# Performance work log

Measured on AMD Instinct MI355X. Metric: run time of the kernel, lower is better.

## Reference

```python
import jax, jax.numpy as jnp
import numpy as np

HEADS = 16
DIM_HEAD = 64


def setup_inputs() -> dict:
    key = jax.random.key(0)
    k1, k2, k3, k4, k5 = jax.random.split(key, 5)
    B, S, E = 4, 2048, 1024
    inner = HEADS * DIM_HEAD  # 1024
    return {
        "hidden_states": jax.random.normal(k1, (B, S, E), dtype=jnp.float32),
        "w_q": jax.random.normal(k2, (E, inner), dtype=jnp.float32) * (E ** -0.5),
        "w_k": jax.random.normal(k3, (E, inner), dtype=jnp.float32) * (E ** -0.5),
        "w_v": jax.random.normal(k4, (E, inner), dtype=jnp.float32) * (E ** -0.5),
        "w_o": jax.random.normal(k5, (inner, E), dtype=jnp.float32) * (inner ** -0.5),
    }


def reference(hidden_states, w_q, w_k, w_v, w_o):
    # Self-attention path: context = hidden_states (context arg is None).
    B, S, _ = hidden_states.shape
    dtype = hidden_states.dtype
    scale = DIM_HEAD ** -0.5

    q = (hidden_states @ w_q).reshape(B, S, HEADS, DIM_HEAD)
    k = (hidden_states @ w_k).reshape(B, S, HEADS, DIM_HEAD)
    v = (hidden_states @ w_v).reshape(B, S, HEADS, DIM_HEAD)

    # fp32 softmax as in the original module
    q32 = q.astype(jnp.float32)
    k32 = k.astype(jnp.float32)
    scores = jnp.einsum('btnh,bfnh->bnft', k32, q32) * scale  # [B, H, S_q, S_kv]
    probs = jax.nn.softmax(scores, axis=-1).astype(dtype)

    out = jnp.einsum('bnft,btnh->bfnh', probs, v)  # [B, S, H, D]
    out = out.reshape(B, S, HEADS * DIM_HEAD)
    return out @ w_o  # [B, S, query_dim]
```

## Files before the change

kernel.cpp:

```cpp
#include <hip/hip_runtime.h>
#include <stdint.h>

typedef __attribute__((ext_vector_type(8))) unsigned short ushort8;
typedef __attribute__((ext_vector_type(8))) __bf16 bf16x8;
typedef __attribute__((ext_vector_type(4))) float f32x4;
typedef __attribute__((ext_vector_type(4))) uint32_t u32x4;

#define TBK 32

__device__ __forceinline__ unsigned short f2bf(float f) {
  union { float f; uint32_t u; } x; x.f = f;
  uint32_t u = x.u;
  uint32_t r = (u + 0x7fffu + ((u >> 16) & 1u)) >> 16;
  return (unsigned short)r;
}

__device__ __forceinline__ uint32_t pack_bf2(float lo, float hi) {
  return (uint32_t)f2bf(lo) | ((uint32_t)f2bf(hi) << 16);
}

__device__ __forceinline__ uint32_t rhu2(float lo, float hi) {
  union { float f; uint32_t u; } a, b; a.f = lo; b.f = hi;
  return __builtin_amdgcn_perm(b.u + 0x8000u, a.u + 0x8000u, 0x07060302u);
}

__device__ __forceinline__ void store_c(unsigned short* p, float v) { *p = f2bf(v); }
__device__ __forceinline__ void store_c(float* p, float v) { *p = v; }

__device__ __forceinline__ void gll16(const unsigned short* g, unsigned short* l) {
  __builtin_amdgcn_global_load_lds((const __attribute__((address_space(1))) void*)g,
                                   (__attribute__((address_space(3))) void*)l,
                                   16, 0, 0);
}

__global__ __launch_bounds__(256) void cvt_f32_bf16(
    const float* __restrict__ x, unsigned short* __restrict__ y, int n4) {
  int i = blockIdx.x * 256 + threadIdx.x;
  if (i >= n4) return;
  float4 v = *(const float4*)(x + (size_t)i * 4);
  uint2 p; p.x = pack_bf2(v.x, v.y); p.y = pack_bf2(v.z, v.w);
  *(uint2*)(y + (size_t)i * 4) = p;
}

__global__ void transpose_w(const float* __restrict__ W,
                            unsigned short* __restrict__ WT) {
  __shared__ unsigned short tile[32][33];
  int c0 = blockIdx.x * 32, r0 = blockIdx.y * 32;
  int x = threadIdx.x, y = threadIdx.y;
#pragma unroll
  for (int i = 0; i < 32; i += 8)
    tile[y + i][x] = f2bf(W[(size_t)(r0 + y + i) * 1024 + c0 + x]);
  __syncthreads();
#pragma unroll
  for (int i = 0; i < 32; i += 8)
    WT[(size_t)(c0 + y + i) * 1024 + r0 + x] = tile[x][y + i];
}

template <typename OutT>
__global__ __launch_bounds__(256) void gemm_bt(
    const unsigned short* A,
    const unsigned short* BT0, const unsigned short* BT1, const unsigned short* BT2,
    OutT* C0, OutT* C1, OutT* C2,
    int M, int N, int K) {
  const unsigned short* BT = (blockIdx.z == 0) ? BT0 : (blockIdx.z == 1) ? BT1 : BT2;
  OutT* C = (blockIdx.z == 0) ? C0 : (blockIdx.z == 1) ? C1 : C2;

  __shared__ __attribute__((aligned(16))) unsigned short As[128 * TBK];
  __shared__ __attribute__((aligned(16))) unsigned short Bs[128 * TBK];

  const int tid = threadIdx.x;
  const int wave = tid >> 6, lane = tid & 63;
  const int fr = lane & 15, fq = lane >> 4;
  const int bm = blockIdx.x * 128, bn = blockIdx.y * 128;
  const int wm = (wave >> 1) * 64, wn = (wave & 1) * 64;

  f32x4 acc[4][4] = {};

  const int sr = lane >> 2;
  const int sk = (lane & 3) * 8;
  const unsigned short* Ag = A + (size_t)(bm + wave * 32 + sr) * K + sk;
  const unsigned short* Bg = BT + (size_t)(bn + wave * 32 + sr) * K + sk;
  unsigned short* As0 = &As[(wave * 32) * TBK];
  unsigned short* Bs0 = &Bs[(wave * 32) * TBK];

  for (int k0 = 0; k0 < K; k0 += TBK) {
    gll16(Ag + k0, As0);
    gll16(Ag + k0 + 16 * K, As0 + 16 * TBK);
    gll16(Bg + k0, Bs0);
    gll16(Bg + k0 + 16 * K, Bs0 + 16 * TBK);
    asm volatile("s_waitcnt vmcnt(0)" ::: "memory");
    __syncthreads();

    bf16x8 af[4], bfr[4];
#pragma unroll
    for (int mt = 0; mt < 4; mt++)
      af[mt] = *(const bf16x8*)&As[(wm + mt * 16 + fr) * TBK + fq * 8];
#pragma unroll
    for (int nt = 0; nt < 4; nt++)
      bfr[nt] = *(const bf16x8*)&Bs[(wn + nt * 16 + fr) * TBK + fq * 8];
#pragma unroll
    for (int mt = 0; mt < 4; mt++)
#pragma unroll
      for (int nt = 0; nt < 4; nt++)
        acc[mt][nt] = __builtin_amdgcn_mfma_f32_16x16x32_bf16(af[mt], bfr[nt], acc[mt][nt], 0, 0, 0);
    __syncthreads();
  }

#pragma unroll
  for (int mt = 0; mt < 4; mt++)
#pragma unroll
    for (int nt = 0; nt < 4; nt++)
#pragma unroll
      for (int r = 0; r < 4; r++) {
        int row = bm + wm + mt * 16 + fq * 4 + r;
        int col = bn + wn + nt * 16 + fr;
        store_c(&C[(size_t)row * N + col], acc[mt][nt][r]);
      }
}

#define SQ 72

__global__ __launch_bounds__(256, 4) void attn_kernel(
    const unsigned short* q, const unsigned short* k,
    const unsigned short* v, unsigned short* o) {
  const int S = 2048, E = 1024;
  __shared__ __attribute__((aligned(16))) unsigned short Ks[64 * SQ];
  __shared__ __attribute__((aligned(16))) unsigned short Vt[64 * SQ];

  const int tid = threadIdx.x;
  const int wave = tid >> 6, lane = tid & 63;
  const int fr = lane & 15, fq = lane >> 4;
  const int q0 = blockIdx.x * 128;
  const int bh = blockIdx.y;
  const int b = bh >> 4, h = bh & 15;
  const size_t base = ((size_t)b * S) * E + (size_t)h * 64;

  bf16x8 aq[2][2];
#pragma unroll
  for (int qg = 0; qg < 2; qg++)
#pragma unroll
    for (int ks = 0; ks < 2; ks++)
      aq[qg][ks] = *(const bf16x8*)&q[base +
          (size_t)(q0 + qg * 64 + wave * 16 + fr) * E + ks * 32 + fq * 8];

  ushort8 ones_u;
#pragma unroll
  for (int j = 0; j < 8; j++) ones_u[j] = 0x3F80;
  bf16x8 onesf = *(bf16x8*)&ones_u;

  f32x4 ot[2][4] = {};
  f32x4 osum[2] = {};
  const float KSC = 0.125f * 1.44269504088896341f;

  const int rp = (tid & 31) * 2;
  const int dcv = (tid >> 5) * 8;
  const int u_ = rp & 31;
  const int slot = 32 * (rp >> 5) + 8 * ((u_ & 15) >> 2) + 4 * (u_ >> 4) + (u_ & 3);

  for (int t0 = 0; t0 < S; t0 += 64) {
    __syncthreads();
#pragma unroll
    for (int i = 0; i < 2; i++) {
      int id = tid + i * 256;
      int row = id >> 3, dc = (id & 7) * 8;
      ushort8 kv = *(const ushort8*)&k[base + (size_t)(t0 + row) * E + dc];
      *(ushort8*)&Ks[row * SQ + dc] = kv;
    }
    {
      u32x4 a = *(const u32x4*)&v[base + (size_t)(t0 + rp) * E + dcv];
      u32x4 bb = *(const u32x4*)&v[base + (size_t)(t0 + rp + 1) * E + dcv];
#pragma unroll
      for (int w = 0; w < 4; w++) {
        uint32_t lo = __builtin_amdgcn_perm(bb[w], a[w], 0x05040100u);
        uint32_t hi = __builtin_amdgcn_perm(bb[w], a[w], 0x07060302u);
        *(uint32_t*)&Vt[(dcv + 2 * w) * SQ + slot] = lo;
        *(uint32_t*)&Vt[(dcv + 2 * w + 1) * SQ + slot] = hi;
      }
    }
    __syncthreads();

    f32x4 st[2][4] = {};
#pragma unroll
    for (int ks = 0; ks < 2; ks++) {
#pragma unroll
      for (int tt = 0; tt < 4; tt++) {
        bf16x8 ak = *(const bf16x8*)&Ks[(tt * 16 + fr) * SQ + ks * 32 + fq * 8];
        st[0][tt] = __builtin_amdgcn_mfma_f32_16x16x32_bf16(ak, aq[0][ks], st[0][tt], 0, 0, 0);
        st[1][tt] = __builtin_amdgcn_mfma_f32_16x16x32_bf16(ak, aq[1][ks], st[1][tt], 0, 0, 0);
      }
    }

    uint32_t pk[2][4][2];
#pragma unroll
    for (int qg = 0; qg < 2; qg++)
#pragma unroll
      for (int tt = 0; tt < 4; tt++) {
        float e0 = __builtin_amdgcn_exp2f(st[qg][tt][0] * KSC);
        float e1 = __builtin_amdgcn_exp2f(st[qg][tt][1] * KSC);
        float e2 = __builtin_amdgcn_exp2f(st[qg][tt][2] * KSC);
        float e3 = __builtin_amdgcn_exp2f(st[qg][tt][3] * KSC);
        pk[qg][tt][0] = rhu2(e0, e1);
        pk[qg][tt][1] = rhu2(e2, e3);
      }

#pragma unroll
    for (int c = 0; c < 2; c++) {
      bf16x8 bp[2];
#pragma unroll
      for (int qg = 0; qg < 2; qg++) {
        u32x4 bpr;
        bpr[0] = pk[qg][2 * c][0];
        bpr[1] = pk[qg][2 * c][1];
        bpr[2] = pk[qg][2 * c + 1][0];
        bpr[3] = pk[qg][2 * c + 1][1];
        bp[qg] = *(bf16x8*)&bpr;
      }
#pragma unroll
      for (int dt = 0; dt < 4; dt++) {
        bf16x8 av = *(const bf16x8*)&Vt[(dt * 16 + fr) * SQ + c * 32 + fq * 8];
        ot[0][dt] = __builtin_amdgcn_mfma_f32_16x16x32_bf16(av, bp[0], ot[0][dt], 0, 0, 0);
        ot[1][dt] = __builtin_amdgcn_mfma_f32_16x16x32_bf16(av, bp[1], ot[1][dt], 0, 0, 0);
      }
      osum[0] = __builtin_amdgcn_mfma_f32_16x16x32_bf16(onesf, bp[0], osum[0], 0, 0, 0);
      osum[1] = __builtin_amdgcn_mfma_f32_16x16x32_bf16(onesf, bp[1], osum[1], 0, 0, 0);
    }
  }

#pragma unroll
  for (int qg = 0; qg < 2; qg++) {
    float inv = 1.0f / osum[qg][0];
    size_t rowbase = base + (size_t)(q0 + qg * 64 + wave * 16 + fr) * E;
#pragma unroll
    for (int dt = 0; dt < 4; dt++) {
      uint32_t w0 = rhu2(ot[qg][dt][0] * inv, ot[qg][dt][1] * inv);
      uint32_t w1 = rhu2(ot[qg][dt][2] * inv, ot[qg][dt][3] * inv);
      *(uint32_t*)&o[rowbase + dt * 16 + fq * 4] = w0;
      *(uint32_t*)&o[rowbase + dt * 16 + fq * 4 + 2] = w1;
    }
  }
}

extern "C" void kernel_launch(void* const* d_in, const int* in_sizes, int n_in,
                              void* d_out, int out_size, void* d_ws, size_t ws_size,
                              hipStream_t stream) {
  const float* hs = (const float*)d_in[0];
  const float* wq = (const float*)d_in[1];
  const float* wk = (const float*)d_in[2];
  const float* wv = (const float*)d_in[3];
  const float* wo = (const float*)d_in[4];
  unsigned short* ws = (unsigned short*)d_ws;

  unsigned short* wqT = ws;
  unsigned short* wkT = ws + 1048576;
  unsigned short* wvT = ws + 2097152;
  unsigned short* woT = wqT;
  unsigned short* qb  = ws + 3145728;
  unsigned short* kb  = qb + 8388608;
  unsigned short* vb  = kb + 8388608;
  unsigned short* ob  = qb;
  unsigned short* hsb = (unsigned short*)d_out;
  float* out = (float*)d_out;

  const int M = 8192, N = 1024, K = 1024;

  cvt_f32_bf16<<<dim3(M * K / 4 / 256), 256, 0, stream>>>(hs, hsb, M * K / 4);

  dim3 tb(32, 8);
  transpose_w<<<dim3(32, 32), tb, 0, stream>>>(wq, wqT);
  transpose_w<<<dim3(32, 32), tb, 0, stream>>>(wk, wkT);
  transpose_w<<<dim3(32, 32), tb, 0, stream>>>(wv, wvT);

  gemm_bt<unsigned short><<<dim3(M / 128, N / 128, 3), 256, 0, stream>>>(
      hsb, wqT, wkT, wvT, qb, kb, vb, M, N, K);

  transpose_w<<<dim3(32, 32), tb, 0, stream>>>(wo, woT);

  attn_kernel<<<dim3(2048 / 128, 64), 256, 0, stream>>>(qb, kb, vb, ob);

  gemm_bt<float><<<dim3(M / 128, N / 128, 1), 256, 0, stream>>>(
      ob, woT, woT, woT, out, out, out, M, N, K);
}
```

Before: 291.8 us.

## Double-buffer attention K/V tiles with async LDS loads and XOR swizzle

The attention kernel now double-buffers K and transposed V tiles in shared memory. It prefetches the next tile (K via direct global-to-LDS loads, V via registers) while computing on the current one, which cuts from two barriers per iteration to one. Padded LDS rows are replaced by an XOR swizzle to avoid bank conflicts. The softmax scale is folded into the Q projection epilogue, which removes a multiply per score element but rounds the scaled Q to bf16.

```diff
diff --git a/kernel.cpp b/kernel.cpp
--- a/kernel.cpp
+++ b/kernel.cpp
@@ -61,9 +61,10 @@
     const unsigned short* A,
     const unsigned short* BT0, const unsigned short* BT1, const unsigned short* BT2,
     OutT* C0, OutT* C1, OutT* C2,
-    int M, int N, int K) {
+    int M, int N, int K, float sc0) {
   const unsigned short* BT = (blockIdx.z == 0) ? BT0 : (blockIdx.z == 1) ? BT1 : BT2;
   OutT* C = (blockIdx.z == 0) ? C0 : (blockIdx.z == 1) ? C1 : C2;
+  const float sc = (blockIdx.z == 0) ? sc0 : 1.0f;
 
   __shared__ __attribute__((aligned(16))) unsigned short As[128 * TBK];
   __shared__ __attribute__((aligned(16))) unsigned short Bs[128 * TBK];
@@ -114,18 +115,16 @@
       for (int r = 0; r < 4; r++) {
         int row = bm + wm + mt * 16 + fq * 4 + r;
         int col = bn + wn + nt * 16 + fr;
-        store_c(&C[(size_t)row * N + col], acc[mt][nt][r]);
-      }
-}
-
-#define SQ 72
+        store_c(&C[(size_t)row * N + col], acc[mt][nt][r] * sc);
+      }
+}
 
 __global__ __launch_bounds__(256, 4) void attn_kernel(
     const unsigned short* q, const unsigned short* k,
     const unsigned short* v, unsigned short* o) {
   const int S = 2048, E = 1024;
-  __shared__ __attribute__((aligned(16))) unsigned short Ks[64 * SQ];
-  __shared__ __attribute__((aligned(16))) unsigned short Vt[64 * SQ];
+  __shared__ __attribute__((aligned(16))) unsigned short Ksb[2 * 64 * 64];
+  __shared__ __attribute__((aligned(16))) unsigned short Vtb[2 * 64 * 64];
 
   const int tid = threadIdx.x;
   const int wave = tid >> 6, lane = tid & 63;
@@ -150,41 +149,57 @@
 
   f32x4 ot[2][4] = {};
   f32x4 osum[2] = {};
-  const float KSC = 0.125f * 1.44269504088896341f;
+
+  const int srow = lane >> 3;
+  const int scol = (((lane & 7) ^ srow) << 3);
+  const unsigned short* Kg = k + base + (size_t)(wave * 16 + srow) * E + scol;
+  unsigned short* KsW0 = &Ksb[wave * 1024];
 
   const int rp = (tid & 31) * 2;
   const int dcv = (tid >> 5) * 8;
   const int u_ = rp & 31;
   const int slot = 32 * (rp >> 5) + 8 * ((u_ & 15) >> 2) + 4 * (u_ >> 4) + (u_ & 3);
-
-  for (int t0 = 0; t0 < S; t0 += 64) {
-    __syncthreads();
-#pragma unroll
-    for (int i = 0; i < 2; i++) {
-      int id = tid + i * 256;
-      int row = id >> 3, dc = (id & 7) * 8;
-      ushort8 kv = *(const ushort8*)&k[base + (size_t)(t0 + row) * E + dc];
-      *(ushort8*)&Ks[row * SQ + dc] = kv;
-    }
-    {
-      u32x4 a = *(const u32x4*)&v[base + (size_t)(t0 + rp) * E + dcv];
-      u32x4 bb = *(const u32x4*)&v[base + (size_t)(t0 + rp + 1) * E + dcv];
-#pragma unroll
-      for (int w = 0; w < 4; w++) {
-        uint32_t lo = __builtin_amdgcn_perm(bb[w], a[w], 0x05040100u);
-        uint32_t hi = __builtin_amdgcn_perm(bb[w], a[w], 0x07060302u);
-        *(uint32_t*)&Vt[(dcv + 2 * w) * SQ + slot] = lo;
-        *(uint32_t*)&Vt[(dcv + 2 * w + 1) * SQ + slot] = hi;
-      }
-    }
-    __syncthreads();
+  const unsigned short* Vg = v + base + (size_t)rp * E + dcv;
+
+  const int rx = (fr & 7) << 3;
+
+  {
+    gll16(Kg, KsW0);
+    gll16(Kg + 8 * (size_t)E, KsW0 + 512);
+    u32x4 a = *(const u32x4*)(Vg);
+    u32x4 bb = *(const u32x4*)(Vg + E);
+#pragma unroll
+    for (int w = 0; w < 4; w++) {
+      uint32_t lo = __builtin_amdgcn_perm(bb[w], a[w], 0x05040100u);
+      uint32_t hi = __builtin_amdgcn_perm(bb[w], a[w], 0x07060302u);
+      int d = dcv + 2 * w;
+      *(uint32_t*)&Vtb[d * 64 + (slot ^ ((2 * w) << 3))] = lo;
+      *(uint32_t*)&Vtb[(d + 1) * 64 + (slot ^ ((2 * w + 1) << 3))] = hi;
+    }
+    asm volatile("s_waitcnt vmcnt(0)" ::: "memory");
+  }
+  __syncthreads();
+
+  int cur = 0;
+  for (int t = 0; t < 32; t++) {
+    const int nxt = cur ^ 4096;
+    const bool pf = (t < 31);
+    u32x4 va, vb;
+    if (pf) {
+      const size_t toff = (size_t)((t + 1) * 64) * E;
+      va = *(const u32x4*)(Vg + toff);
+      vb = *(const u32x4*)(Vg + toff + E);
+      gll16(Kg + toff, &Ksb[nxt + wave * 1024]);
+      gll16(Kg + toff + 8 * (size_t)E, &Ksb[nxt + wave * 1024 + 512]);
+    }
 
     f32x4 st[2][4] = {};
 #pragma unroll
     for (int ks = 0; ks < 2; ks++) {
 #pragma unroll
       for (int tt = 0; tt < 4; tt++) {
-        bf16x8 ak = *(const bf16x8*)&Ks[(tt * 16 + fr) * SQ + ks * 32 + fq * 8];
+        bf16x8 ak = *(const bf16x8*)&Ksb[cur + (tt * 16 + fr) * 64 +
+                                         ((ks * 32 + fq * 8) ^ rx)];
         st[0][tt] = __builtin_amdgcn_mfma_f32_16x16x32_bf16(ak, aq[0][ks], st[0][tt], 0, 0, 0);
         st[1][tt] = __builtin_amdgcn_mfma_f32_16x16x32_bf16(ak, aq[1][ks], st[1][tt], 0, 0, 0);
       }
@@ -195,13 +210,24 @@
     for (int qg = 0; qg < 2; qg++)
 #pragma unroll
       for (int tt = 0; tt < 4; tt++) {
-        float e0 = __builtin_amdgcn_exp2f(st[qg][tt][0] * KSC);
-        float e1 = __builtin_amdgcn_exp2f(st[qg][tt][1] * KSC);
-        float e2 = __builtin_amdgcn_exp2f(st[qg][tt][2] * KSC);
-        float e3 = __builtin_amdgcn_exp2f(st[qg][tt][3] * KSC);
+        float e0 = __builtin_amdgcn_exp2f(st[qg][tt][0]);
+        float e1 = __builtin_amdgcn_exp2f(st[qg][tt][1]);
+        float e2 = __builtin_amdgcn_exp2f(st[qg][tt][2]);
+        float e3 = __builtin_amdgcn_exp2f(st[qg][tt][3]);
         pk[qg][tt][0] = rhu2(e0, e1);
         pk[qg][tt][1] = rhu2(e2, e3);
       }
+
+    if (pf) {
+#pragma unroll
+      for (int w = 0; w < 4; w++) {
+        uint32_t lo = __builtin_amdgcn_perm(vb[w], va[w], 0x05040100u);
+        uint32_t hi = __builtin_amdgcn_perm(vb[w], va[w], 0x07060302u);
+        int d = dcv + 2 * w;
+        *(uint32_t*)&Vtb[nxt + d * 64 + (slot ^ ((2 * w) << 3))] = lo;
+        *(uint32_t*)&Vtb[nxt + (d + 1) * 64 + (slot ^ ((2 * w + 1) << 3))] = hi;
+      }
+    }
 
 #pragma unroll
     for (int c = 0; c < 2; c++) {
@@ -217,13 +243,18 @@
       }
 #pragma unroll
       for (int dt = 0; dt < 4; dt++) {
-        bf16x8 av = *(const bf16x8*)&Vt[(dt * 16 + fr) * SQ + c * 32 + fq * 8];
+        bf16x8 av = *(const bf16x8*)&Vtb[cur + (dt * 16 + fr) * 64 +
+                                         ((c * 32 + fq * 8) ^ rx)];
         ot[0][dt] = __builtin_amdgcn_mfma_f32_16x16x32_bf16(av, bp[0], ot[0][dt], 0, 0, 0);
         ot[1][dt] = __builtin_amdgcn_mfma_f32_16x16x32_bf16(av, bp[1], ot[1][dt], 0, 0, 0);
       }
       osum[0] = __builtin_amdgcn_mfma_f32_16x16x32_bf16(onesf, bp[0], osum[0], 0, 0, 0);
       osum[1] = __builtin_amdgcn_mfma_f32_16x16x32_bf16(onesf, bp[1], osum[1], 0, 0, 0);
     }
+
+    if (pf) asm volatile("s_waitcnt vmcnt(0)" ::: "memory");
+    __syncthreads();
+    cur = nxt;
   }
 
 #pragma unroll
@@ -262,6 +293,7 @@
   float* out = (float*)d_out;
 
   const int M = 8192, N = 1024, K = 1024;
+  const float KSC = 0.125f * 1.44269504088896341f;
 
   cvt_f32_bf16<<<dim3(M * K / 4 / 256), 256, 0, stream>>>(hs, hsb, M * K / 4);
 
@@ -271,12 +303,12 @@
   transpose_w<<<dim3(32, 32), tb, 0, stream>>>(wv, wvT);
 
   gemm_bt<unsigned short><<<dim3(M / 128, N / 128, 3), 256, 0, stream>>>(
-      hsb, wqT, wkT, wvT, qb, kb, vb, M, N, K);
+      hsb, wqT, wkT, wvT, qb, kb, vb, M, N, K, KSC);
 
   transpose_w<<<dim3(32, 32), tb, 0, stream>>>(wo, woT);
 
   attn_kernel<<<dim3(2048 / 128, 64), 256, 0, stream>>>(qb, kb, vb, ob);
 
   gemm_bt<float><<<dim3(M / 128, N / 128, 1), 256, 0, stream>>>(
-      ob, woT, woT, woT, out, out, out, M, N, K);
-}
+      ob, woT, woT, woT, out, out, out, M, N, K, 1.0f);
+}
```

New measurement: 296.8 us. Within noise of the previous version (+1.7%).
